# Kernel optimization log

Hardware: AMD Instinct MI355X
Metric: run time of the kernel (lower is better)

The kernel has to match this reference:

```python
import jax, jax.numpy as jnp
import numpy as np

B = 4
MAX_N = 2048
D = 512
H = 8
HD = D // H
SRC_LENS = [2048, 1536, 1800, 1200]   # sum = 6584
REF_LENS = [1900, 2048, 1400, 1600]   # sum = 6948
NEG_INF = -1e9


def setup_inputs() -> dict:
    key = jax.random.key(0)
    ks = jax.random.split(key, 8)
    n_src, n_ref = sum(SRC_LENS), sum(REF_LENS)
    s = 0.02
    return {
        "feats_src": jax.random.normal(ks[0], (n_src, D), dtype=jnp.float32),
        "batch_src": jnp.asarray(np.repeat(np.arange(B), SRC_LENS), dtype=jnp.int32),
        "feats_ref": jax.random.normal(ks[1], (n_ref, D), dtype=jnp.float32),
        "batch_ref": jnp.asarray(np.repeat(np.arange(B), REF_LENS), dtype=jnp.int32),
        "w_in": jax.random.normal(ks[2], (3 * D, D), dtype=jnp.float32) * s,
        "b_in": jnp.zeros((3 * D,), dtype=jnp.float32),
        "w_out": jax.random.normal(ks[3], (D, D), dtype=jnp.float32) * s,
        "b_out": jnp.zeros((D,), dtype=jnp.float32),
        "gw1": jax.random.normal(ks[4], (D, D), dtype=jnp.float32) * s,
        "gb1": jnp.zeros((D,), dtype=jnp.float32),
        "gw2": jax.random.normal(ks[5], (1, D), dtype=jnp.float32) * s,
        "gb2": jnp.zeros((1,), dtype=jnp.float32),
    }


def _to_dense(feats, batch_idx):
    # sparse [N, D] (sorted batch indices) -> dense [B, MAX_N, D] + key_padding_mask
    n = feats.shape[0]
    counts = jax.ops.segment_sum(jnp.ones((n,), jnp.int32), batch_idx, num_segments=B)
    starts = jnp.concatenate([jnp.zeros((1,), jnp.int32), jnp.cumsum(counts)[:-1].astype(jnp.int32)])
    pos = jnp.arange(n, dtype=jnp.int32) - starts[batch_idx]  # position within batch
    dense = jnp.zeros((B, MAX_N, feats.shape[1]), feats.dtype).at[batch_idx, pos].set(feats)
    mask = jnp.arange(MAX_N)[None, :] >= counts[:, None]  # True = padding (key_padding_mask)
    return dense, mask, pos


def reference(feats_src, batch_src, feats_ref, batch_ref,
              w_in, b_in, w_out, b_out, gw1, gb1, gw2, gb2):
    d_src, mask_src, pos_src = _to_dense(feats_src, batch_src)
    d_ref, mask_ref, _ = _to_dense(feats_ref, batch_ref)

    # nn.MultiheadAttention (batch_first, eval mode): packed in_proj, scaled dot-product
    q = (d_src @ w_in[:D].T + b_in[:D]).reshape(B, MAX_N, H, HD)
    k = (d_ref @ w_in[D:2 * D].T + b_in[D:2 * D]).reshape(B, MAX_N, H, HD)
    v = (d_ref @ w_in[2 * D:].T + b_in[2 * D:]).reshape(B, MAX_N, H, HD)
    scores = jnp.einsum('bqhd,bkhd->bhqk', q * (HD ** -0.5), k)
    scores = jnp.where(mask_ref[:, None, None, :], NEG_INF, scores)
    attn = jax.nn.softmax(scores, axis=-1)
    ctx = jnp.einsum('bhqk,bkhd->bqhd', attn, v).reshape(B, MAX_N, D)
    d_aligned = ctx @ w_out.T + b_out

    # gate MLP: Linear -> ReLU -> Linear -> Sigmoid
    gate = jax.nn.sigmoid(jax.nn.relu(d_aligned @ gw1.T + gb1) @ gw2.T + gb2)  # [B, MAX_N, 1]
    d_out = d_src + gate * d_aligned

    # dense -> ragged: gather each token back to its flat slot
    out_flat = d_out[batch_src, pos_src]  # [N_src, D]
    return out_flat, gate
```

## Files before the change

### kernel.cpp

```cpp
#include <hip/hip_runtime.h>
#include <hip/hip_bf16.h>


typedef __bf16 bf16x8_t __attribute__((ext_vector_type(8)));
typedef __bf16 bf16x4_t __attribute__((ext_vector_type(4)));
typedef float f32x4_t __attribute__((ext_vector_type(4)));
typedef float f32x2_t __attribute__((ext_vector_type(2)));

#define CQ_SCALE 0.18033688011112042f

__device__ inline bf16x8_t zero8() {
  bf16x8_t z;
#pragma unroll
  for (int t = 0; t < 8; ++t) z[t] = (__bf16)0.0f;
  return z;
}

__device__ __forceinline__ int sniff_f32(const void* w) {
  unsigned short u = ((const unsigned short*)w)[threadIdx.x & 63];
  return __ballot((u & 0x7F80) >= 0x3F80) != 0ULL;
}

__device__ __forceinline__ int2 swz(int bid, int nwg, int nby) {
  int chunk = nwg >> 3;
  int w = (bid & 7) * chunk + (bid >> 3);
  return make_int2(w / nby, w % nby);
}

__global__ void sentinel_k(float* out) {
  if (threadIdx.x == 0 && blockIdx.x == 0) out[0] = 1000.0f;
}

__global__ void cv_all(const void* w_in, const void* b_in, const void* w_out,
                       const void* b_out, const void* gw1, const void* gb1,
                       const void* gw2, const void* gb2,
                       __hip_bfloat16* __restrict__ ws,
                       const void* fs, const void* fr, int do_feats) {
  int f = sniff_f32(w_in);
  int bid = blockIdx.x;
  if (do_feats && bid < 3383) {
    int i = bid * 256 + threadIdx.x;
    const int NFS = 421376;
    const void* src;
    size_t dst;
    int off;
    if (i < NFS) { src = fs; dst = 11803680; off = i * 8; }
    else { src = fr; dst = 15174688; off = (i - NFS) * 8; }
    __hip_bfloat16* d = ws + dst + off;
    if (f) {
      const float* p = (const float*)src + off;
      bf16x8_t v;
#pragma unroll
      for (int e = 0; e < 8; ++e) v[e] = (__bf16)p[e];
      *reinterpret_cast<bf16x8_t*>(d) = v;
    } else {
      *reinterpret_cast<bf16x8_t*>(d) =
          *reinterpret_cast<const bf16x8_t*>((const __hip_bfloat16*)src + off);
    }
    return;
  }
  int base = do_feats ? 3383 : 0;
  int nb = gridDim.x - base;
  const size_t F_W_IN = 16, F_B_IN = 786448, F_W_OUT = 787984, F_B_OUT = 1050128,
               F_GW1 = 1050640, F_GB1 = 1312784, F_GW2 = 1313296, F_GB2 = 1313808;
  const int total = 1313793;
  for (int g = (bid - base) * 256 + threadIdx.x; g < total; g += nb * 256) {
    const void* src;
    size_t dst;
    int i;
    if (g < 786432) { src = w_in; dst = F_W_IN; i = g; }
    else if (g < 787968) { src = b_in; dst = F_B_IN; i = g - 786432; }
    else if (g < 1050112) { src = w_out; dst = F_W_OUT; i = g - 787968; }
    else if (g < 1050624) { src = b_out; dst = F_B_OUT; i = g - 1050112; }
    else if (g < 1312768) { src = gw1; dst = F_GW1; i = g - 1050624; }
    else if (g < 1313280) { src = gb1; dst = F_GB1; i = g - 1312768; }
    else if (g < 1313792) { src = gw2; dst = F_GW2; i = g - 1313280; }
    else { src = gb2; dst = F_GB2; i = g - 1313792; }
    ws[dst + i] = f ? __float2bfloat16(((const float*)src)[i])
                    : ((const __hip_bfloat16*)src)[i];
  }
}

__device__ __forceinline__ void gemm_core(
    const void* __restrict__ A_, long aoff, const __hip_bfloat16* __restrict__ Bt,
    const __hip_bfloat16* __restrict__ bias, __hip_bfloat16* __restrict__ C,
    int M, int K, int lda, int ldc, float cscale, int relu, int f, int bm, int bn,
    long chs, __bf16 (&As)[128][72], __bf16 (&Bs)[128][72]) {
  int tid = threadIdx.x, lane = tid & 63, wave = tid >> 6;
  int wm = wave >> 1, wn = wave & 1;
  int l15 = lane & 15, quad = lane >> 4;

  f32x4_t acc[4][4];
#pragma unroll
  for (int i = 0; i < 4; ++i)
#pragma unroll
    for (int j = 0; j < 4; ++j)
#pragma unroll
      for (int r = 0; r < 4; ++r) acc[i][j][r] = 0.f;

  bf16x8_t ra[4], rb[4];
  f32x4_t raf[4][2];

  auto gload = [&](int k0) {
#pragma unroll
    for (int s = 0; s < 4; ++s) {
      int id = s * 256 + tid;
      int row = id >> 3, col = (id & 7) * 8;
      int arow = bm + row;
      if (f) {
        if (arow < M) {
          const float* p = (const float*)A_ + aoff + (size_t)arow * lda + k0 + col;
          raf[s][0] = *reinterpret_cast<const f32x4_t*>(p);
          raf[s][1] = *reinterpret_cast<const f32x4_t*>(p + 4);
        } else {
#pragma unroll
          for (int e = 0; e < 4; ++e) { raf[s][0][e] = 0.f; raf[s][1][e] = 0.f; }
        }
      } else {
        ra[s] = (arow < M)
                    ? *reinterpret_cast<const bf16x8_t*>((const __hip_bfloat16*)A_ + aoff +
                                                         (size_t)arow * lda + k0 + col)
                    : zero8();
      }
      rb[s] = *reinterpret_cast<const bf16x8_t*>(Bt + (size_t)(bn + row) * 512 + k0 + col);
    }
  };
  auto stage = [&]() {
#pragma unroll
    for (int s = 0; s < 4; ++s) {
      int id = s * 256 + tid;
      int row = id >> 3, col = (id & 7) * 8;
      if (f) {
        bf16x8_t t;
#pragma unroll
        for (int e = 0; e < 4; ++e) {
          t[e] = (__bf16)raf[s][0][e];
          t[4 + e] = (__bf16)raf[s][1][e];
        }
        *reinterpret_cast<bf16x8_t*>(&As[row][col]) = t;
      } else {
        *reinterpret_cast<bf16x8_t*>(&As[row][col]) = ra[s];
      }
      *reinterpret_cast<bf16x8_t*>(&Bs[row][col]) = rb[s];
    }
  };

  int nk = K >> 6;
  gload(0);
  for (int it = 0; it < nk; ++it) {
    stage();
    __syncthreads();
    if (it + 1 < nk) gload((it + 1) * 64);
#pragma unroll
    for (int ks = 0; ks < 2; ++ks) {
      bf16x8_t af[4], bfv[4];
#pragma unroll
      for (int i = 0; i < 4; ++i)
        af[i] = *reinterpret_cast<const bf16x8_t*>(
            &As[wm * 64 + i * 16 + l15][ks * 32 + quad * 8]);
#pragma unroll
      for (int j = 0; j < 4; ++j)
        bfv[j] = *reinterpret_cast<const bf16x8_t*>(
            &Bs[wn * 64 + j * 16 + l15][ks * 32 + quad * 8]);
#pragma unroll
      for (int i = 0; i < 4; ++i)
#pragma unroll
        for (int j = 0; j < 4; ++j)
          acc[i][j] = __builtin_amdgcn_mfma_f32_16x16x32_bf16(af[i], bfv[j], acc[i][j], 0, 0, 0);
    }
    __syncthreads();
  }

#pragma unroll
  for (int i = 0; i < 4; ++i)
#pragma unroll
    for (int j = 0; j < 4; ++j) {
      int col = bn + wn * 64 + j * 16 + l15;
      float bv = __bfloat162float(bias[col]);
#pragma unroll
      for (int r = 0; r < 4; ++r) {
        int row = bm + wm * 64 + i * 16 + quad * 4 + r;
        if (row < M) {
          float v = (acc[i][j][r] + bv) * cscale;
          if (relu) v = fmaxf(v, 0.f);
          size_t idx = chs ? ((size_t)(col >> 6) * chs + (size_t)row * 64 + (col & 63))
                           : ((size_t)row * ldc + col);
          C[idx] = __float2bfloat16(v);
        }
      }
    }
}

__global__ __launch_bounds__(256) void proj2(
    const void* __restrict__ fs, const void* __restrict__ fr,
    const __hip_bfloat16* __restrict__ ws, __hip_bfloat16* __restrict__ Q,
    __hip_bfloat16* __restrict__ KV, const void* snf) {
  __shared__ __bf16 As[128][72];
  __shared__ __bf16 Bs[128][72];
  const size_t F_W_IN = 16, F_B_IN = 786448;
  const long CHS = (long)6948 * 64;
  int f = snf ? sniff_f32(snf) : 0;
  int bid = blockIdx.x;
  if (bid < 208) {
    int2 s = swz(bid, 208, 4);
    gemm_core(fs, 0, ws + F_W_IN, ws + F_B_IN, Q, 6584, 512, 512, 512, CQ_SCALE, 0, f,
              s.x * 128, s.y * 128, 0, As, Bs);
  } else {
    int2 s = swz(bid - 208, 440, 8);
    gemm_core(fr, 0, ws + F_W_IN + 262144, ws + F_B_IN + 512, KV, 6948, 512, 512, 1024,
              1.0f, 0, f, s.x * 128, s.y * 128, CHS, As, Bs);
  }
}

__global__ __launch_bounds__(256) void gemm128z(
    const __hip_bfloat16* __restrict__ A, const __hip_bfloat16* __restrict__ Bt,
    const __hip_bfloat16* __restrict__ bias, __hip_bfloat16* __restrict__ C,
    int M, float cscale, int relu) {
  __shared__ __bf16 As[128][72];
  __shared__ __bf16 Bs[128][72];
  int2 s = swz(blockIdx.x, gridDim.x, 4);
  gemm_core(A, 0, Bt, bias, C, M, 512, 512, 512, cscale, relu, 0,
            s.x * 128, s.y * 128, 0, As, Bs);
}

template <bool AF32>
__global__ __launch_bounds__(256) void gemm128(
    const void* __restrict__ A_, long aoff, const __hip_bfloat16* __restrict__ Bt,
    const __hip_bfloat16* __restrict__ bias, __hip_bfloat16* __restrict__ C,
    int M, int K, int lda, int ldc, float cscale, int relu, long chs,
    const void* snf) {
  __shared__ __bf16 As[128][72];
  __shared__ __bf16 Bs[128][72];
  int f = 0;
  if constexpr (AF32) f = sniff_f32(snf);
  gemm_core(A_, aoff, Bt, bias, C, M, K, lda, ldc, cscale, relu, f,
            blockIdx.x * 128, blockIdx.y * 128, chs, As, Bs);
}

template <int NS>
__global__ __launch_bounds__(256) void gemm128_pv(
    const __hip_bfloat16* __restrict__ P, const float* __restrict__ L,
    const __hip_bfloat16* __restrict__ Bt, const __hip_bfloat16* __restrict__ bias,
    __hip_bfloat16* __restrict__ C, int M) {
  const size_t PSZ = 3375104;
  __shared__ __bf16 As[128][72];
  __shared__ __bf16 Bs[128][72];
  int tid = threadIdx.x, lane = tid & 63, wave = tid >> 6;
  int wm = wave >> 1, wn = wave & 1;
  int l15 = lane & 15, quad = lane >> 4;
  int2 sw = swz(blockIdx.x, 208, 4);
  int bm = sw.x * 128, bn = sw.y * 128;

  f32x4_t acc[4][4];
#pragma unroll
  for (int i = 0; i < 4; ++i)
#pragma unroll
    for (int j = 0; j < 4; ++j)
#pragma unroll
      for (int r = 0; r < 4; ++r) acc[i][j][r] = 0.f;

  bf16x8_t rp[NS][4], rb[4];
  float rl[4][NS];

  auto gload = [&](int k0) {
    int h = k0 >> 6;
#pragma unroll
    for (int s = 0; s < 4; ++s) {
      int id = s * 256 + tid;
      int row = id >> 3, col = (id & 7) * 8;
      int arow = bm + row;
      if (arow < M) {
        size_t off = (size_t)arow * 512 + k0 + col;
#pragma unroll
        for (int i = 0; i < NS; ++i)
          rp[i][s] = *reinterpret_cast<const bf16x8_t*>(P + i * PSZ + off);
        const float* lp = &L[((size_t)arow * 8 + h) * NS];
#pragma unroll
        for (int i = 0; i < NS; ++i) rl[s][i] = lp[i];
      } else {
#pragma unroll
        for (int i = 0; i < NS; ++i) rp[i][s] = zero8();
        rl[s][0] = 1.f;
#pragma unroll
        for (int i = 1; i < NS; ++i) rl[s][i] = 0.f;
      }
      rb[s] = *reinterpret_cast<const bf16x8_t*>(Bt + (size_t)(bn + row) * 512 + k0 + col);
    }
  };
  auto stage = [&]() {
#pragma unroll
    for (int s = 0; s < 4; ++s) {
      int id = s * 256 + tid;
      int row = id >> 3, col = (id & 7) * 8;
      float sum = 0.f;
#pragma unroll
      for (int i = 0; i < NS; ++i) sum += rl[s][i];
      float sc = 1.0f / sum;
      bf16x8_t t;
#pragma unroll
      for (int e = 0; e < 8; ++e) {
        float v = 0.f;
#pragma unroll
        for (int i = 0; i < NS; ++i) v += rl[s][i] * (float)rp[i][s][e];
        t[e] = (__bf16)(v * sc);
      }
      *reinterpret_cast<bf16x8_t*>(&As[row][col]) = t;
      *reinterpret_cast<bf16x8_t*>(&Bs[row][col]) = rb[s];
    }
  };

  gload(0);
  for (int it = 0; it < 8; ++it) {
    stage();
    __syncthreads();
    if (it + 1 < 8) gload((it + 1) * 64);
#pragma unroll
    for (int ks = 0; ks < 2; ++ks) {
      bf16x8_t af[4], bfv[4];
#pragma unroll
      for (int i = 0; i < 4; ++i)
        af[i] = *reinterpret_cast<const bf16x8_t*>(
            &As[wm * 64 + i * 16 + l15][ks * 32 + quad * 8]);
#pragma unroll
      for (int j = 0; j < 4; ++j)
        bfv[j] = *reinterpret_cast<const bf16x8_t*>(
            &Bs[wn * 64 + j * 16 + l15][ks * 32 + quad * 8]);
#pragma unroll
      for (int i = 0; i < 4; ++i)
#pragma unroll
        for (int j = 0; j < 4; ++j)
          acc[i][j] = __builtin_amdgcn_mfma_f32_16x16x32_bf16(af[i], bfv[j], acc[i][j], 0, 0, 0);
    }
    __syncthreads();
  }

#pragma unroll
  for (int i = 0; i < 4; ++i)
#pragma unroll
    for (int j = 0; j < 4; ++j) {
      int col = bn + wn * 64 + j * 16 + l15;
      float bv = __bfloat162float(bias[col]);
#pragma unroll
      for (int r = 0; r < 4; ++r) {
        int row = bm + wm * 64 + i * 16 + quad * 4 + r;
        if (row < M)
          C[(size_t)row * 512 + col] = __float2bfloat16(acc[i][j][r] + bv);
      }
    }
}

__device__ __forceinline__ void flash_core(
    const __hip_bfloat16* __restrict__ Qb, const __hip_bfloat16* __restrict__ Kb,
    const __hip_bfloat16* __restrict__ Vb, __hip_bfloat16* __restrict__ OUTb,
    float* __restrict__ LPb, int lns, int nsrc, int nref, int qt, int kt0,
    int ktNfull, int do_tail, __bf16 (&KsL)[2][64][68], __bf16 (&VtL)[2][64][72],
    __bf16 (&PL)[4][32][68]) {
  int h = blockIdx.y;
  int tid = threadIdx.x, lane = tid & 63, wave = tid >> 6;
  int l15 = lane & 15, quad = lane >> 4;
  int Mb = nsrc + 1;
  int qbase = qt * 128 + wave * 32;

  bf16x8_t qfr[2][2];
#pragma unroll
  for (int g = 0; g < 2; ++g) {
    int qrow = qbase + g * 16 + l15;
#pragma unroll
    for (int ks = 0; ks < 2; ++ks)
      qfr[g][ks] = (qrow < nsrc)
                       ? *reinterpret_cast<const bf16x8_t*>(
                             Qb + (size_t)qrow * 512 + h * 64 + ks * 32 + quad * 8)
                       : zero8();
  }

  f32x4_t O[2][4];
#pragma unroll
  for (int g = 0; g < 2; ++g)
#pragma unroll
    for (int j = 0; j < 4; ++j)
#pragma unroll
      for (int r = 0; r < 4; ++r) O[g][j][r] = 0.f;

  f32x4_t Lacc[2];
#pragma unroll
  for (int g = 0; g < 2; ++g)
#pragma unroll
    for (int r = 0; r < 4; ++r) Lacc[g][r] = 0.f;
  bf16x8_t ones;
#pragma unroll
  for (int t = 0; t < 8; ++t) ones[t] = (__bf16)1.0f;

  auto load64pair = [&](const __bf16* p) {
    bf16x4_t lo = *reinterpret_cast<const bf16x4_t*>(p);
    bf16x4_t hi = *reinterpret_cast<const bf16x4_t*>(p + 4);
    bf16x8_t v;
#pragma unroll
    for (int e = 0; e < 4; ++e) {
      v[e] = lo[e];
      v[4 + e] = hi[e];
    }
    return v;
  };

  bf16x8_t krA[2], v0, v1;
  auto gloadK = [&](int k0) {
    const __hip_bfloat16* base = Kb + (size_t)k0 * 64 + tid * 16;
    krA[0] = *reinterpret_cast<const bf16x8_t*>(base);
    krA[1] = *reinterpret_cast<const bf16x8_t*>(base + 8);
  };
  auto stageK = [&](int buf) {
#pragma unroll
    for (int p = 0; p < 2; ++p) {
      int lin = tid * 16 + p * 8;
      int row = lin >> 6, col = lin & 63;
      *reinterpret_cast<bf16x4_t*>(&KsL[buf][row][col]) =
          *reinterpret_cast<const bf16x4_t*>(&krA[p]);
      bf16x4_t hi;
#pragma unroll
      for (int e = 0; e < 4; ++e) hi[e] = krA[p][4 + e];
      *reinterpret_cast<bf16x4_t*>(&KsL[buf][row][col + 4]) = hi;
    }
  };
  auto loadV = [&](int k0) {
    const __hip_bfloat16* vp = Vb + (size_t)(k0 + lane) * 64 + wave * 16;
    v0 = *reinterpret_cast<const bf16x8_t*>(vp);
    v1 = *reinterpret_cast<const bf16x8_t*>(vp + 8);
  };

  int nit = ktNfull - kt0;
  if (nit > 0) {
    gloadK(kt0 * 64);
    loadV(kt0 * 64);
  }

  int buf = 0;
  for (int it = 0; it < nit; ++it) {
    int k0 = (kt0 + it) * 64;
    stageK(buf);
    {
      __bf16(*Vt)[72] = VtL[buf];
#pragma unroll
      for (int e = 0; e < 8; ++e) {
        Vt[wave * 16 + e][lane] = v0[e];
        Vt[wave * 16 + 8 + e][lane] = v1[e];
      }
    }
    __syncthreads();
    if (it + 1 < nit) {
      gloadK(k0 + 64);
      loadV(k0 + 64);
    }

    bf16x8_t kf[8];
#pragma unroll
    for (int j = 0; j < 4; ++j)
#pragma unroll
      for (int ks = 0; ks < 2; ++ks)
        kf[j * 2 + ks] = load64pair(&KsL[buf][j * 16 + l15][ks * 32 + quad * 8]);
#pragma unroll
    for (int g = 0; g < 2; ++g) {
      f32x4_t St[4];
#pragma unroll
      for (int j = 0; j < 4; ++j)
#pragma unroll
        for (int r = 0; r < 4; ++r) St[j][r] = 0.f;
#pragma unroll
      for (int j = 0; j < 4; ++j)
#pragma unroll
        for (int ks = 0; ks < 2; ++ks)
          St[j] = __builtin_amdgcn_mfma_f32_16x16x32_bf16(kf[j * 2 + ks], qfr[g][ks],
                                                          St[j], 0, 0, 0);
#pragma unroll
      for (int j = 0; j < 4; ++j) {
        bf16x4_t pk;
#pragma unroll
        for (int r = 0; r < 4; ++r) pk[r] = (__bf16)exp2f(St[j][r]);
        *reinterpret_cast<bf16x4_t*>(&PL[wave][g * 16 + l15][j * 16 + quad * 4]) = pk;
      }
    }

    bf16x8_t pa[2][2];
#pragma unroll
    for (int g = 0; g < 2; ++g)
#pragma unroll
      for (int ks = 0; ks < 2; ++ks)
        pa[g][ks] = load64pair(&PL[wave][g * 16 + l15][ks * 32 + quad * 8]);
#pragma unroll
    for (int g = 0; g < 2; ++g)
#pragma unroll
      for (int ks = 0; ks < 2; ++ks)
        Lacc[g] = __builtin_amdgcn_mfma_f32_16x16x32_bf16(pa[g][ks], ones, Lacc[g], 0, 0, 0);
#pragma unroll
    for (int j = 0; j < 4; ++j)
#pragma unroll
      for (int ks = 0; ks < 2; ++ks) {
        bf16x8_t vbf = *reinterpret_cast<const bf16x8_t*>(
            &VtL[buf][j * 16 + l15][ks * 32 + quad * 8]);
#pragma unroll
        for (int g = 0; g < 2; ++g)
          O[g][j] = __builtin_amdgcn_mfma_f32_16x16x32_bf16(pa[g][ks], vbf, O[g][j], 0, 0, 0);
      }
    __syncthreads();
    buf ^= 1;
  }

  if (do_tail) {
    int k0 = ktNfull * 64;
    __bf16(*Vt)[72] = VtL[buf];
    {
      int kr = k0 + lane;
      const __hip_bfloat16* vp = Vb + (size_t)kr * 64 + wave * 16;
      bf16x8_t t0 = (kr < nref) ? *reinterpret_cast<const bf16x8_t*>(vp) : zero8();
      bf16x8_t t1 = (kr < nref) ? *reinterpret_cast<const bf16x8_t*>(vp + 8) : zero8();
#pragma unroll
      for (int e = 0; e < 8; ++e) {
        Vt[wave * 16 + e][lane] = t0[e];
        Vt[wave * 16 + 8 + e][lane] = t1[e];
      }
    }
    bf16x8_t kf[8];
#pragma unroll
    for (int j = 0; j < 4; ++j) {
      int kcol = k0 + j * 16 + l15;
      const __hip_bfloat16* kp = Kb + (size_t)kcol * 64 + quad * 8;
      kf[j * 2] = (kcol < nref) ? *reinterpret_cast<const bf16x8_t*>(kp) : zero8();
      kf[j * 2 + 1] = (kcol < nref) ? *reinterpret_cast<const bf16x8_t*>(kp + 32) : zero8();
    }
#pragma unroll
    for (int g = 0; g < 2; ++g) {
      f32x4_t St[4];
#pragma unroll
      for (int j = 0; j < 4; ++j)
#pragma unroll
        for (int r = 0; r < 4; ++r) St[j][r] = 0.f;
#pragma unroll
      for (int j = 0; j < 4; ++j)
#pragma unroll
        for (int ks = 0; ks < 2; ++ks)
          St[j] = __builtin_amdgcn_mfma_f32_16x16x32_bf16(kf[j * 2 + ks], qfr[g][ks],
                                                          St[j], 0, 0, 0);
#pragma unroll
      for (int j = 0; j < 4; ++j) {
        bf16x4_t pk;
#pragma unroll
        for (int r = 0; r < 4; ++r) {
          int kl = k0 + j * 16 + quad * 4 + r;
          pk[r] = (__bf16)((kl < nref) ? exp2f(St[j][r]) : 0.f);
        }
        *reinterpret_cast<bf16x4_t*>(&PL[wave][g * 16 + l15][j * 16 + quad * 4]) = pk;
      }
    }
    __syncthreads();
    bf16x8_t pa[2][2];
#pragma unroll
    for (int g = 0; g < 2; ++g)
#pragma unroll
      for (int ks = 0; ks < 2; ++ks)
        pa[g][ks] = load64pair(&PL[wave][g * 16 + l15][ks * 32 + quad * 8]);
#pragma unroll
    for (int g = 0; g < 2; ++g)
#pragma unroll
      for (int ks = 0; ks < 2; ++ks)
        Lacc[g] = __builtin_amdgcn_mfma_f32_16x16x32_bf16(pa[g][ks], ones, Lacc[g], 0, 0, 0);
#pragma unroll
    for (int j = 0; j < 4; ++j)
#pragma unroll
      for (int ks = 0; ks < 2; ++ks) {
        bf16x8_t vbf =
            *reinterpret_cast<const bf16x8_t*>(&Vt[j * 16 + l15][ks * 32 + quad * 8]);
#pragma unroll
        for (int g = 0; g < 2; ++g)
          O[g][j] = __builtin_amdgcn_mfma_f32_16x16x32_bf16(pa[g][ks], vbf, O[g][j], 0, 0, 0);
      }
  }

  if (LPb && l15 == 0) {
#pragma unroll
    for (int g = 0; g < 2; ++g)
#pragma unroll
      for (int r = 0; r < 4; ++r) {
        int row = qbase + g * 16 + quad * 4 + r;
        if (row < Mb) LPb[((size_t)row * 8 + h) * lns] = Lacc[g][r];
      }
  }

#pragma unroll
  for (int g = 0; g < 2; ++g)
#pragma unroll
    for (int r = 0; r < 4; ++r) {
      int row = qbase + g * 16 + quad * 4 + r;
      if (row < Mb) {
        float inv = 1.0f / Lacc[g][r];
#pragma unroll
        for (int j = 0; j < 4; ++j)
          OUTb[(size_t)row * 512 + h * 64 + j * 16 + l15] =
              __float2bfloat16(O[g][j][r] * inv);
      }
    }
}

__global__ __launch_bounds__(256, 3) void flash_all(
    const __hip_bfloat16* __restrict__ Q, const __hip_bfloat16* __restrict__ KV,
    __hip_bfloat16* __restrict__ P, float* __restrict__ L, int nsplit) {
  const int TILE_START[4] = {0, 17, 30, 45};
  const int SRC_START[4] = {0, 2048, 3584, 5384};
  const int REF_START[4] = {0, 1900, 3948, 5348};
  const int SRC_LEN[4] = {2048, 1536, 1800, 1200};
  const int REF_LEN[4] = {1900, 2048, 1400, 1600};
  const int CS[4] = {0, 2049, 3586, 5387};
  const size_t PSZ = 3375104;
  const size_t CHS = (size_t)6948 * 64;
  __shared__ __bf16 KsL[2][64][68];
  __shared__ __bf16 VtL[2][64][72];
  __shared__ __bf16 PL[4][32][68];
  int bid = blockIdx.x;
  int b = (bid >= TILE_START[3]) ? 3 : (bid >= TILE_START[2]) ? 2 : (bid >= TILE_START[1]) ? 1 : 0;
  int qt = bid - TILE_START[b];
  int nref = REF_LEN[b];
  int full = nref >> 6, nkt = (nref + 63) >> 6, rem = nref & 63;
  int split = blockIdx.z;
  int kt0 = (nkt * split) / nsplit;
  int ktN, tail;
  if (split == nsplit - 1) { ktN = full; tail = rem > 0; }
  else { ktN = (nkt * (split + 1)) / nsplit; tail = 0; }
  int h = blockIdx.y;
  const __hip_bfloat16* Kb = KV + (size_t)h * CHS + (size_t)REF_START[b] * 64;
  const __hip_bfloat16* Vb = KV + (size_t)(8 + h) * CHS + (size_t)REF_START[b] * 64;
  __hip_bfloat16* OUT = P + (size_t)split * PSZ;
  float* LP = (nsplit == 1) ? nullptr : (L + split + (size_t)CS[b] * 8 * nsplit);
  flash_core(Q + (size_t)SRC_START[b] * 512, Kb, Vb, OUT + (size_t)CS[b] * 512, LP,
             nsplit, SRC_LEN[b], nref, qt, kt0, ktN, tail, KsL, VtL, PL);
}

__global__ __launch_bounds__(256, 3) void flash_one(const __hip_bfloat16* __restrict__ Qb,
                                                    const __hip_bfloat16* __restrict__ KVb,
                                                    __hip_bfloat16* __restrict__ OUTb,
                                                    int nsrc, int nref, long chs) {
  __shared__ __bf16 KsL[2][64][68];
  __shared__ __bf16 VtL[2][64][72];
  __shared__ __bf16 PL[4][32][68];
  int h = blockIdx.y;
  const __hip_bfloat16* Kb = KVb + (size_t)h * chs;
  const __hip_bfloat16* Vb = KVb + (size_t)(8 + h) * chs;
  flash_core(Qb, Kb, Vb, OUTb, nullptr, 1, nsrc, nref, blockIdx.x, 0, nref >> 6,
             (nref & 63) > 0, KsL, VtL, PL);
}

__global__ __launch_bounds__(256) void finalize_all(
    const void* __restrict__ src, const __hip_bfloat16* __restrict__ aligned,
    const __hip_bfloat16* __restrict__ hidden, const __hip_bfloat16* __restrict__ gw2,
    const __hip_bfloat16* __restrict__ gb2, void* __restrict__ out, const void* snf) {
  int f = sniff_f32(snf);
  int lane = threadIdx.x & 63;
  int r = blockIdx.x * 4 + (threadIdx.x >> 6);
  int b = (r >= 5387) ? 3 : (r >= 3586) ? 2 : (r >= 2049) ? 1 : 0;
  const int CS[4] = {0, 2049, 3586, 5387};
  const int NSRC[4] = {2048, 1536, 1800, 1200};
  int pos = r - CS[b];
  int c0 = lane * 8;

  bf16x8_t hv = *reinterpret_cast<const bf16x8_t*>(hidden + (size_t)r * 512 + c0);
  bf16x8_t wv = *reinterpret_cast<const bf16x8_t*>(gw2 + c0);
  float zacc = 0.f;
#pragma unroll
  for (int e = 0; e < 8; ++e)
    zacc += __bfloat162float(hv[e]) * __bfloat162float(wv[e]);
  for (int o = 32; o; o >>= 1) zacc += __shfl_xor(zacc, o);
  zacc += __bfloat162float(gb2[0]);
  float g = 1.f / (1.f + __expf(-zacc));

  const size_t GOFF = (size_t)6584 * 512;
  if (pos < NSRC[b]) {
    size_t ib = (size_t)(r - b) * 512 + c0;
    bf16x8_t av = *reinterpret_cast<const bf16x8_t*>(aligned + (size_t)r * 512 + c0);
    if (f) {
      const float* sp = (const float*)src + ib;
      f32x4_t s0 = *reinterpret_cast<const f32x4_t*>(sp);
      f32x4_t s1 = *reinterpret_cast<const f32x4_t*>(sp + 4);
      f32x4_t o0, o1;
#pragma unroll
      for (int e = 0; e < 4; ++e) {
        o0[e] = s0[e] + g * __bfloat162float(av[e]);
        o1[e] = s1[e] + g * __bfloat162float(av[4 + e]);
      }
      float* op = (float*)out + ib;
      *reinterpret_cast<f32x4_t*>(op) = o0;
      *reinterpret_cast<f32x4_t*>(op + 4) = o1;
    } else {
      bf16x8_t sv = *reinterpret_cast<const bf16x8_t*>((const __hip_bfloat16*)src + ib);
      bf16x8_t ov;
#pragma unroll
      for (int e = 0; e < 8; ++e)
        ov[e] = (__bf16)(__bfloat162float(sv[e]) + g * __bfloat162float(av[e]));
      *reinterpret_cast<bf16x8_t*>((__hip_bfloat16*)out + ib) = ov;
    }
    if (lane == 0) {
      size_t go = GOFF + b * 2048 + pos;
      if (f) ((float*)out)[go] = g;
      else ((__hip_bfloat16*)out)[go] = __float2bfloat16(g);
    }
  } else {
    for (int p = NSRC[b] + lane; p < 2048; p += 64) {
      size_t go = GOFF + b * 2048 + p;
      if (f) ((float*)out)[go] = g;
      else ((__hip_bfloat16*)out)[go] = __float2bfloat16(g);
    }
  }
}

__global__ __launch_bounds__(256) void finalize_b(
    const void* __restrict__ src, const __hip_bfloat16* __restrict__ alnb,
    const __hip_bfloat16* __restrict__ hidb, const __hip_bfloat16* __restrict__ gw2,
    const __hip_bfloat16* __restrict__ gb2, void* __restrict__ out,
    int b, int nsrc, int src_start, const void* snf) {
  int f = sniff_f32(snf);
  int lane = threadIdx.x & 63;
  int r = blockIdx.x * 4 + (threadIdx.x >> 6);
  if (r > nsrc) return;

  float zacc = 0.f;
  const __hip_bfloat16* hrow = hidb + (size_t)r * 512;
#pragma unroll
  for (int t = 0; t < 8; ++t) {
    int c = lane + (t << 6);
    zacc += __bfloat162float(hrow[c]) * __bfloat162float(gw2[c]);
  }
  for (int o = 32; o; o >>= 1) zacc += __shfl_xor(zacc, o);
  zacc += __bfloat162float(gb2[0]);
  float g = 1.f / (1.f + __expf(-zacc));

  const size_t GOFF = (size_t)6584 * 512;
  if (r < nsrc) {
    size_t ib = (size_t)(src_start + r) * 512;
    const __hip_bfloat16* arow = alnb + (size_t)r * 512;
#pragma unroll
    for (int t = 0; t < 8; ++t) {
      int c = lane + (t << 6);
      float sv = f ? ((const float*)src)[ib + c]
                   : __bfloat162float(((const __hip_bfloat16*)src)[ib + c]);
      float val = sv + g * __bfloat162float(arow[c]);
      if (f) ((float*)out)[ib + c] = val;
      else ((__hip_bfloat16*)out)[ib + c] = __float2bfloat16(val);
    }
    if (lane == 0) {
      size_t go = GOFF + b * 2048 + r;
      if (f) ((float*)out)[go] = g;
      else ((__hip_bfloat16*)out)[go] = __float2bfloat16(g);
    }
  } else {
    for (int p = nsrc + lane; p < 2048; p += 64) {
      size_t go = GOFF + b * 2048 + p;
      if (f) ((float*)out)[go] = g;
      else ((__hip_bfloat16*)out)[go] = __float2bfloat16(g);
    }
  }
}

extern "C" void kernel_launch(void* const* d_in, const int* in_sizes, int n_in,
                              void* d_out, int out_size, void* d_ws, size_t ws_size,
                              hipStream_t stream) {
  (void)in_sizes; (void)n_in; (void)out_size;
  const void* feats_src = d_in[0];
  const void* feats_ref = d_in[2];
  const void* w_in = d_in[4];
  const void* b_in = d_in[5];
  const void* w_out = d_in[6];
  const void* b_out = d_in[7];
  const void* gw1 = d_in[8];
  const void* gb1 = d_in[9];
  const void* gw2 = d_in[10];
  const void* gb2 = d_in[11];

  const size_t F_W_IN = 16, F_B_IN = 786448, F_W_OUT = 787984, F_B_OUT = 1050128,
               F_GW1 = 1050640, F_GB1 = 1312784, F_GW2 = 1313296, F_GB2 = 1313808,
               A0 = 1313824;
  const size_t PSZ = 3375104;
  const size_t R3E = A0 + PSZ + 7114752;
  const size_t FS0 = R3E;
  const size_t FR0 = R3E + 3371008;
  const size_t NEED_A2 = 2 * (R3E + 2 * PSZ + 210816);
  const size_t NEED_A = 2 * (R3E + PSZ);
  const size_t NEED_B = 2 * (A0 + 4259840);

  if (ws_size < NEED_B) {
    sentinel_k<<<1, 64, 0, stream>>>((float*)d_out);
    return;
  }

  __hip_bfloat16* ws = (__hip_bfloat16*)d_ws;

  const int SRC_LEN[4] = {2048, 1536, 1800, 1200};
  const int REF_LEN[4] = {1900, 2048, 1400, 1600};
  const int SRC_START[4] = {0, 2048, 3584, 5384};
  const int REF_START[4] = {0, 1900, 3948, 5348};
  dim3 blk(256);

  if (ws_size >= NEED_A) {
    __hip_bfloat16* R1 = ws + A0;
    __hip_bfloat16* R2 = R1 + PSZ;
    __hip_bfloat16* R3 = R2 + 7114752;
    int NS = (ws_size >= NEED_A2) ? 2 : 1;
    if (NS == 2) {
      cv_all<<<dim3(4407), blk, 0, stream>>>(w_in, b_in, w_out, b_out, gw1, gb1,
                                             gw2, gb2, ws, feats_src, feats_ref, 1);
      proj2<<<dim3(648), blk, 0, stream>>>(ws + FS0, ws + FR0, ws, R1, R2, nullptr);
      float* L = (float*)(ws + R3E + 2 * PSZ);
      flash_all<<<dim3(55, 8, 2), blk, 0, stream>>>(R1, R2, R3, L, 2);
      gemm128_pv<2><<<dim3(208), blk, 0, stream>>>(R3, L, ws + F_W_OUT,
                                                   ws + F_B_OUT, R1, 6588);
    } else {
      cv_all<<<dim3(1024), blk, 0, stream>>>(w_in, b_in, w_out, b_out, gw1, gb1,
                                             gw2, gb2, ws, nullptr, nullptr, 0);
      proj2<<<dim3(648), blk, 0, stream>>>(feats_src, feats_ref, ws, R1, R2, w_in);
      flash_all<<<dim3(55, 8, 1), blk, 0, stream>>>(R1, R2, R3, nullptr, 1);
      gemm128z<<<dim3(208), blk, 0, stream>>>(R3, ws + F_W_OUT, ws + F_B_OUT, R1,
                                              6588, 1.0f, 0);
    }
    gemm128z<<<dim3(208), blk, 0, stream>>>(R1, ws + F_GW1, ws + F_GB1, R3, 6588,
                                            1.0f, 1);
    finalize_all<<<dim3(1647), blk, 0, stream>>>(feats_src, R1, R3, ws + F_GW2,
                                                 ws + F_GB2, d_out, w_in);
  } else {
    cv_all<<<dim3(1024), blk, 0, stream>>>(w_in, b_in, w_out, b_out, gw1, gb1,
                                           gw2, gb2, ws, nullptr, nullptr, 0);
    __hip_bfloat16* W2 = ws + A0;
    __hip_bfloat16* W1 = W2 + 2097152;
    __hip_bfloat16* W3 = W1 + 1081344;
    const long CHS_B = (long)2048 * 64;
    for (int b = 0; b < 4; ++b) {
      int nsrc = SRC_LEN[b], nref = REF_LEN[b];
      gemm128<true><<<dim3((nsrc + 127) / 128, 4), blk, 0, stream>>>(
          feats_src, (long)SRC_START[b] * 512, ws + F_W_IN, ws + F_B_IN, W1, nsrc, 512,
          512, 512, CQ_SCALE, 0, 0, w_in);
      gemm128<true><<<dim3((nref + 127) / 128, 8), blk, 0, stream>>>(
          feats_ref, (long)REF_START[b] * 512, ws + F_W_IN + 262144, ws + F_B_IN + 512,
          W2, nref, 512, 512, 1024, 1.0f, 0, CHS_B, w_in);
      flash_one<<<dim3((nsrc + 128) / 128, 8), blk, 0, stream>>>(W1, W2, W3, nsrc, nref,
                                                                 CHS_B);
      gemm128<false><<<dim3((nsrc + 128) / 128, 4), blk, 0, stream>>>(
          W3, 0, ws + F_W_OUT, ws + F_B_OUT, W1, nsrc + 1, 512, 512, 512, 1.0f, 0, 0,
          nullptr);
      gemm128<false><<<dim3((nsrc + 128) / 128, 4), blk, 0, stream>>>(
          W1, 0, ws + F_GW1, ws + F_GB1, W3, nsrc + 1, 512, 512, 512, 1.0f, 1, 0,
          nullptr);
      finalize_b<<<dim3((nsrc + 4) / 4), blk, 0, stream>>>(
          feats_src, W1, W3, ws + F_GW2, ws + F_GB2, d_out, b, nsrc, SRC_START[b], w_in);
    }
  }
}
```

Baseline: 239.7 us.

## Fuse gate MLP second layer into first gate GEMM epilogue; split flash launches

Adds a gate_gemm kernel that computes the first gate layer, applies ReLU and dots each row with gw2 in the epilogue. It writes per-column-tile partial gate logits to a small float buffer instead of storing the full bf16 hidden activation. finalize_all now sums four partials rather than rereading a 512-wide hidden row, which cuts memory traffic. Separately, the two-way KV-split flash launch becomes two sequential launches, one per split, which may lose concurrency between the splits.

```diff
diff --git a/kernel.cpp b/kernel.cpp
--- a/kernel.cpp
+++ b/kernel.cpp
@@ -237,6 +237,114 @@
             blockIdx.x * 128, blockIdx.y * 128, chs, As, Bs);
 }
 
+__global__ __launch_bounds__(256) void gate_gemm(
+    const __hip_bfloat16* __restrict__ A, const __hip_bfloat16* __restrict__ Bt,
+    const __hip_bfloat16* __restrict__ bias, const __hip_bfloat16* __restrict__ gw2,
+    float* __restrict__ z4, int M) {
+  __shared__ __bf16 As[128][72];
+  __shared__ __bf16 Bs[128][72];
+  __shared__ float zsc[128][2];
+  int tid = threadIdx.x, lane = tid & 63, wave = tid >> 6;
+  int wm = wave >> 1, wn = wave & 1;
+  int l15 = lane & 15, quad = lane >> 4;
+  int2 sw = swz(blockIdx.x, 208, 4);
+  int bm = sw.x * 128, bn = sw.y * 128;
+
+  f32x4_t acc[4][4];
+#pragma unroll
+  for (int i = 0; i < 4; ++i)
+#pragma unroll
+    for (int j = 0; j < 4; ++j)
+#pragma unroll
+      for (int r = 0; r < 4; ++r) acc[i][j][r] = 0.f;
+
+  bf16x8_t ra[4], rb[4];
+  auto gload = [&](int k0) {
+#pragma unroll
+    for (int s = 0; s < 4; ++s) {
+      int id = s * 256 + tid;
+      int row = id >> 3, col = (id & 7) * 8;
+      int arow = bm + row;
+      ra[s] = (arow < M)
+                  ? *reinterpret_cast<const bf16x8_t*>(A + (size_t)arow * 512 + k0 + col)
+                  : zero8();
+      rb[s] = *reinterpret_cast<const bf16x8_t*>(Bt + (size_t)(bn + row) * 512 + k0 + col);
+    }
+  };
+  auto stage = [&]() {
+#pragma unroll
+    for (int s = 0; s < 4; ++s) {
+      int id = s * 256 + tid;
+      int row = id >> 3, col = (id & 7) * 8;
+      *reinterpret_cast<bf16x8_t*>(&As[row][col]) = ra[s];
+      *reinterpret_cast<bf16x8_t*>(&Bs[row][col]) = rb[s];
+    }
+  };
+
+  gload(0);
+  for (int it = 0; it < 8; ++it) {
+    stage();
+    __syncthreads();
+    if (it + 1 < 8) gload((it + 1) * 64);
+#pragma unroll
+    for (int ks = 0; ks < 2; ++ks) {
+      bf16x8_t af[4], bfv[4];
+#pragma unroll
+      for (int i = 0; i < 4; ++i)
+        af[i] = *reinterpret_cast<const bf16x8_t*>(
+            &As[wm * 64 + i * 16 + l15][ks * 32 + quad * 8]);
+#pragma unroll
+      for (int j = 0; j < 4; ++j)
+        bfv[j] = *reinterpret_cast<const bf16x8_t*>(
+            &Bs[wn * 64 + j * 16 + l15][ks * 32 + quad * 8]);
+#pragma unroll
+      for (int i = 0; i < 4; ++i)
+#pragma unroll
+        for (int j = 0; j < 4; ++j)
+          acc[i][j] = __builtin_amdgcn_mfma_f32_16x16x32_bf16(af[i], bfv[j], acc[i][j], 0, 0, 0);
+    }
+    __syncthreads();
+  }
+
+  float zp[4][4];
+#pragma unroll
+  for (int i = 0; i < 4; ++i)
+#pragma unroll
+    for (int r = 0; r < 4; ++r) zp[i][r] = 0.f;
+#pragma unroll
+  for (int i = 0; i < 4; ++i)
+#pragma unroll
+    for (int j = 0; j < 4; ++j) {
+      int col = bn + wn * 64 + j * 16 + l15;
+      float bv = __bfloat162float(bias[col]);
+      float w2 = __bfloat162float(gw2[col]);
+#pragma unroll
+      for (int r = 0; r < 4; ++r) {
+        float v = fmaxf(acc[i][j][r] + bv, 0.f);
+        zp[i][r] += v * w2;
+      }
+    }
+#pragma unroll
+  for (int i = 0; i < 4; ++i)
+#pragma unroll
+    for (int r = 0; r < 4; ++r) {
+#pragma unroll
+      for (int o = 1; o <= 8; o <<= 1) zp[i][r] += __shfl_xor(zp[i][r], o);
+    }
+  if (l15 == 0) {
+#pragma unroll
+    for (int i = 0; i < 4; ++i)
+#pragma unroll
+      for (int r = 0; r < 4; ++r)
+        zsc[wm * 64 + i * 16 + quad * 4 + r][wn] = zp[i][r];
+  }
+  __syncthreads();
+  if (tid < 128) {
+    int row = bm + tid;
+    if (row < M) z4[sw.y * 6592 + row] = zsc[tid][0] + zsc[tid][1];
+  }
+}
+
 template <int NS>
 __global__ __launch_bounds__(256) void gemm128_pv(
     const __hip_bfloat16* __restrict__ P, const float* __restrict__ L,
@@ -601,7 +709,7 @@
 
 __global__ __launch_bounds__(256, 3) void flash_all(
     const __hip_bfloat16* __restrict__ Q, const __hip_bfloat16* __restrict__ KV,
-    __hip_bfloat16* __restrict__ P, float* __restrict__ L, int nsplit) {
+    __hip_bfloat16* __restrict__ P, float* __restrict__ L, int zbase, int nsplit) {
   const int TILE_START[4] = {0, 17, 30, 45};
   const int SRC_START[4] = {0, 2048, 3584, 5384};
   const int REF_START[4] = {0, 1900, 3948, 5348};
@@ -618,7 +726,7 @@
   int qt = bid - TILE_START[b];
   int nref = REF_LEN[b];
   int full = nref >> 6, nkt = (nref + 63) >> 6, rem = nref & 63;
-  int split = blockIdx.z;
+  int split = zbase;
   int kt0 = (nkt * split) / nsplit;
   int ktN, tail;
   if (split == nsplit - 1) { ktN = full; tail = rem > 0; }
@@ -648,8 +756,8 @@
 
 __global__ __launch_bounds__(256) void finalize_all(
     const void* __restrict__ src, const __hip_bfloat16* __restrict__ aligned,
-    const __hip_bfloat16* __restrict__ hidden, const __hip_bfloat16* __restrict__ gw2,
-    const __hip_bfloat16* __restrict__ gb2, void* __restrict__ out, const void* snf) {
+    const float* __restrict__ z4, const __hip_bfloat16* __restrict__ gb2,
+    void* __restrict__ out, const void* snf) {
   int f = sniff_f32(snf);
   int lane = threadIdx.x & 63;
   int r = blockIdx.x * 4 + (threadIdx.x >> 6);
@@ -659,15 +767,9 @@
   int pos = r - CS[b];
   int c0 = lane * 8;
 
-  bf16x8_t hv = *reinterpret_cast<const bf16x8_t*>(hidden + (size_t)r * 512 + c0);
-  bf16x8_t wv = *reinterpret_cast<const bf16x8_t*>(gw2 + c0);
-  float zacc = 0.f;
-#pragma unroll
-  for (int e = 0; e < 8; ++e)
-    zacc += __bfloat162float(hv[e]) * __bfloat162float(wv[e]);
-  for (int o = 32; o; o >>= 1) zacc += __shfl_xor(zacc, o);
-  zacc += __bfloat162float(gb2[0]);
-  float g = 1.f / (1.f + __expf(-zacc));
+  float z = z4[r] + z4[6592 + r] + z4[2 * 6592 + r] + z4[3 * 6592 + r] +
+            __bfloat162float(gb2[0]);
+  float g = 1.f / (1.f + __expf(-z));
 
   const size_t GOFF = (size_t)6584 * 512;
   if (pos < NSRC[b]) {
@@ -778,8 +880,9 @@
   const size_t R3E = A0 + PSZ + 7114752;
   const size_t FS0 = R3E;
   const size_t FR0 = R3E + 3371008;
-  const size_t NEED_A2 = 2 * (R3E + 2 * PSZ + 210816);
-  const size_t NEED_A = 2 * (R3E + PSZ);
+  const size_t Z4EL = 52736;
+  const size_t NEED_A2 = 2 * (R3E + 2 * PSZ + 210816 + Z4EL);
+  const size_t NEED_A = 2 * (R3E + PSZ + Z4EL);
   const size_t NEED_B = 2 * (A0 + 4259840);
 
   if (ws_size < NEED_B) {
@@ -801,25 +904,32 @@
     __hip_bfloat16* R3 = R2 + 7114752;
     int NS = (ws_size >= NEED_A2) ? 2 : 1;
     if (NS == 2) {
+      float* L = (float*)(ws + R3E + 2 * PSZ);
+      float* Z4 = (float*)(ws + R3E + 2 * PSZ + 210816);
       cv_all<<<dim3(4407), blk, 0, stream>>>(w_in, b_in, w_out, b_out, gw1, gb1,
                                              gw2, gb2, ws, feats_src, feats_ref, 1);
       proj2<<<dim3(648), blk, 0, stream>>>(ws + FS0, ws + FR0, ws, R1, R2, nullptr);
-      float* L = (float*)(ws + R3E + 2 * PSZ);
-      flash_all<<<dim3(55, 8, 2), blk, 0, stream>>>(R1, R2, R3, L, 2);
+      flash_all<<<dim3(55, 8, 1), blk, 0, stream>>>(R1, R2, R3, L, 0, 2);
+      flash_all<<<dim3(55, 8, 1), blk, 0, stream>>>(R1, R2, R3, L, 1, 2);
       gemm128_pv<2><<<dim3(208), blk, 0, stream>>>(R3, L, ws + F_W_OUT,
                                                    ws + F_B_OUT, R1, 6588);
+      gate_gemm<<<dim3(208), blk, 0, stream>>>(R1, ws + F_GW1, ws + F_GB1,
+                                               ws + F_GW2, Z4, 6588);
+      finalize_all<<<dim3(1647), blk, 0, stream>>>(feats_src, R1, Z4, ws + F_GB2,
+                                                   d_out, w_in);
     } else {
+      float* Z4 = (float*)(ws + R3E + PSZ);
       cv_all<<<dim3(1024), blk, 0, stream>>>(w_in, b_in, w_out, b_out, gw1, gb1,
                                              gw2, gb2, ws, nullptr, nullptr, 0);
       proj2<<<dim3(648), blk, 0, stream>>>(feats_src, feats_ref, ws, R1, R2, w_in);
-      flash_all<<<dim3(55, 8, 1), blk, 0, stream>>>(R1, R2, R3, nullptr, 1);
+      flash_all<<<dim3(55, 8, 1), blk, 0, stream>>>(R1, R2, R3, nullptr, 0, 1);
       gemm128z<<<dim3(208), blk, 0, stream>>>(R3, ws + F_W_OUT, ws + F_B_OUT, R1,
                                               6588, 1.0f, 0);
-    }
-    gemm128z<<<dim3(208), blk, 0, stream>>>(R1, ws + F_GW1, ws + F_GB1, R3, 6588,
-                                            1.0f, 1);
-    finalize_all<<<dim3(1647), blk, 0, stream>>>(feats_src, R1, R3, ws + F_GW2,
-                                                 ws + F_GB2, d_out, w_in);
+      gate_gemm<<<dim3(208), blk, 0, stream>>>(R1, ws + F_GW1, ws + F_GB1,
+                                               ws + F_GW2, Z4, 6588);
+      finalize_all<<<dim3(1647), blk, 0, stream>>>(feats_src, R1, Z4, ws + F_GB2,
+                                                   d_out, w_in);
+    }
   } else {
     cv_all<<<dim3(1024), blk, 0, stream>>>(w_in, b_in, w_out, b_out, gw1, gb1,
                                            gw2, gb2, ws, nullptr, nullptr, 0);
```

New measurement: 252.9 us. +5.5%, slower.
